# Optimization experiments

Hardware: AMD Instinct MI355X
Metric: run time of the kernel (lower is better)

The kernel has to match this reference:

```python
import jax, jax.numpy as jnp
import numpy as np

E = 1024   # n_embd
H = 16     # n_heads
D = 64     # head_dim
G = 4      # n_kv_groups
F = 4096   # ffn hidden_dim
V = 32000  # vocab
L = 4      # n_layers (all full_attention)
B = 1
T = 2048
ROT = 16   # partial_rotary_factor 0.25 * head_dim 64, rounded to even
EPS = 1e-6
THETA = 10000.0


def rope_tables(seq_len):
    # matches compute_rope_params: inv_freq over even indices of rotary_dim
    inv_freq = 1.0 / (THETA ** (jnp.arange(0, ROT, 2, dtype=jnp.float32) / ROT))
    ang = jnp.arange(seq_len, dtype=jnp.float32)[:, None] * inv_freq[None, :]
    ang = jnp.concatenate([ang, ang], axis=1)  # [T, ROT]
    return jnp.cos(ang), jnp.sin(ang)


def rmsnorm(x, w):
    # torch RMSNorm: x * rsqrt(mean(x^2)+eps) * (1 + weight)
    xf = x.astype(jnp.float32)
    n = xf * jax.lax.rsqrt(jnp.mean(xf * xf, axis=-1, keepdims=True) + EPS)
    return (n * (1.0 + w)).astype(x.dtype)


def apply_rope(x, cos, sin):
    # x: [B, h, T, D]; cos/sin: [1, 1, T, ROT]; partial rotary on first ROT dims
    x_rot, x_pass = x[..., :ROT], x[..., ROT:]
    x1, x2 = x_rot[..., :ROT // 2], x_rot[..., ROT // 2:]
    rotated = jnp.concatenate([-x2, x1], axis=-1)
    return jnp.concatenate([x_rot * cos + rotated * sin, x_pass], axis=-1)


def _forward(tokens, emb, Wq, Wk, Wv, Wo, qn, kn, n1, n2, f1, f2, f3, fn, head):
    cos, sin = rope_tables(T)
    cos = cos[None, None]  # [1,1,T,ROT]
    sin = sin[None, None]
    mask = jnp.triu(jnp.ones((T, T), dtype=bool), k=1)  # True = masked
    scale = D ** -0.5
    x = emb[tokens]  # [B,T,E]

    def block(x, p):
        wq, wk, wv, wo, qw, kw, w1, w2, g1, g2, g3 = p
        h = rmsnorm(x, w1)
        # fused Q + gate projection -> [B,T,H,2D], chunk on last dim
        qg = (h @ wq).reshape(B, T, H, 2 * D)
        q = qg[..., :D].transpose(0, 2, 1, 3)            # [B,H,T,D]
        gate = qg[..., D:].reshape(B, T, H * D)          # [B,T,H*D]
        k = (h @ wk).reshape(B, T, G, D).transpose(0, 2, 1, 3)  # [B,G,T,D]
        v = (h @ wv).reshape(B, T, G, D).transpose(0, 2, 1, 3)
        q = rmsnorm(q, qw)
        k = rmsnorm(k, kw)
        q = apply_rope(q, cos, sin)
        k = apply_rope(k, cos, sin)
        k = jnp.repeat(k, H // G, axis=1)  # GQA expand -> [B,H,T,D]
        v = jnp.repeat(v, H // G, axis=1)
        scores = jnp.einsum('bhqd,bhkd->bhqk', q, k)
        scores = jnp.where(mask, -jnp.inf, scores) * scale
        w = jax.nn.softmax(scores.astype(jnp.float32), axis=-1).astype(q.dtype)
        ctx = jnp.einsum('bhqk,bhkd->bhqd', w, v)
        ctx = ctx.transpose(0, 2, 1, 3).reshape(B, T, H * D)
        ctx = ctx * jax.nn.sigmoid(gate)
        x = x + ctx @ wo
        h2 = rmsnorm(x, w2)
        ff = (jax.nn.silu(h2 @ g1) * (h2 @ g2)) @ g3
        return x + ff, None

    params = (Wq, Wk, Wv, Wo, qn, kn, n1, n2, f1, f2, f3)
    x, _ = jax.lax.scan(block, x, params)
    return rmsnorm(x, fn) @ head  # logits [B,T,V]


def setup_inputs() -> dict:
    key = jax.random.key(0)
    ks = jax.random.split(key, 16)
    s = 0.02
    rn = lambda k, shape, sc=s: jax.random.normal(k, shape, jnp.float32) * sc
    return {
        'tokens': jax.random.randint(ks[0], (B, T), 0, V),
        'emb': rn(ks[1], (V, E)),
        'Wq': rn(ks[2], (L, E, 2 * H * D)),
        'Wk': rn(ks[3], (L, E, G * D)),
        'Wv': rn(ks[4], (L, E, G * D)),
        'Wo': rn(ks[5], (L, H * D, E)),
        'qn': rn(ks[6], (L, D)),
        'kn': rn(ks[7], (L, D)),
        'n1': rn(ks[8], (L, E)),
        'n2': rn(ks[9], (L, E)),
        'f1': rn(ks[10], (L, E, F)),
        'f2': rn(ks[11], (L, E, F)),
        'f3': rn(ks[12], (L, F, E)),
        'fn': rn(ks[13], (E,)),
        'head': rn(ks[14], (E, V)),
    }


def reference(tokens, emb, Wq, Wk, Wv, Wo, qn, kn, n1, n2, f1, f2, f3, fn, head):
    return _forward(tokens, emb, Wq, Wk, Wv, Wo, qn, kn, n1, n2, f1, f2, f3, fn, head)
```

## Files before the change

kernel.cpp:

```cpp
#include <hip/hip_runtime.h>

#define T_LEN 2048
#define E_DIM 1024
#define H_N 16
#define G_N 4
#define D_H 64
#define F_DIM 4096
#define V_SZ 32000
#define L_N 4

typedef __attribute__((ext_vector_type(8))) __bf16 bf16x8;
typedef __attribute__((ext_vector_type(4))) float f32x4;

__device__ __forceinline__ unsigned short f2bf(float f){
  unsigned int u = __float_as_uint(f);
  unsigned int r = (u + 0x7FFFu + ((u >> 16) & 1u)) >> 16;
  return (unsigned short)r;
}

__device__ __forceinline__ f32x4 mfma16(bf16x8 a, bf16x8 b, f32x4 c){
  return __builtin_amdgcn_mfma_f32_16x16x32_bf16(a, b, c, 0, 0, 0);
}

__device__ __forceinline__ void gl16(const void* g, void* l){
  __builtin_amdgcn_global_load_lds((const __attribute__((address_space(1))) void*)g,
                                   (__attribute__((address_space(3))) void*)l, 16, 0, 0);
}

#define SBAR() __builtin_amdgcn_s_barrier()
#define LGK0() do{ asm volatile("s_waitcnt lgkmcnt(0)" ::: "memory"); __builtin_amdgcn_sched_barrier(0); }while(0)
#define VMC4() do{ asm volatile("s_waitcnt vmcnt(4)" ::: "memory"); __builtin_amdgcn_sched_barrier(0); }while(0)
#define VMC0() do{ asm volatile("s_waitcnt vmcnt(0)" ::: "memory"); __builtin_amdgcn_sched_barrier(0); }while(0)

#define QSCALE 0.1803368801111183f

__global__ __launch_bounds__(256) void embed_k(const float* __restrict__ emb,
                                               const int* __restrict__ tokens,
                                               float* __restrict__ x){
  int t = blockIdx.x;
  int tok = tokens[t];
  const float4* src = (const float4*)(emb + (size_t)tok * E_DIM);
  float4* dst = (float4*)(x + (size_t)t * E_DIM);
  dst[threadIdx.x] = src[threadIdx.x];
}

__global__ __launch_bounds__(256) void transpose_bf16(const float* __restrict__ src,
                                                      unsigned short* __restrict__ dst,
                                                      int R, int C){
  __shared__ float tile[32][33];
  int c0 = blockIdx.x * 32, r0 = blockIdx.y * 32;
  int tx = threadIdx.x & 31, ty = threadIdx.x >> 5;
  for (int i = 0; i < 4; i++){
    int r = ty + i * 8;
    tile[r][tx] = src[(size_t)(r0 + r) * C + c0 + tx];
  }
  __syncthreads();
  for (int i = 0; i < 4; i++){
    int r = ty + i * 8;
    dst[(size_t)(c0 + r) * R + r0 + tx] = f2bf(tile[tx][r]);
  }
}

__device__ __forceinline__ void tr32(const float* __restrict__ src, unsigned short* __restrict__ dst,
                                     int R, int C, int bx, int by, float* tile ){
  int c0 = bx * 32, r0 = by * 32;
  int tx = threadIdx.x & 31, ty = threadIdx.x >> 5;
  for (int i = 0; i < 4; i++){
    int r = ty + i * 8;
    tile[r * 33 + tx] = src[(size_t)(r0 + r) * C + c0 + tx];
  }
  __syncthreads();
  for (int i = 0; i < 4; i++){
    int r = ty + i * 8;
    dst[(size_t)(c0 + r) * R + r0 + tx] = f2bf(tile[tx * 33 + r]);
  }
}

__global__ __launch_bounds__(256) void prep_weights(const float* __restrict__ Wq, const float* __restrict__ Wk,
                                                    const float* __restrict__ Wv, const float* __restrict__ Wo,
                                                    const float* __restrict__ f1, const float* __restrict__ f2,
                                                    const float* __restrict__ f3,
                                                    unsigned short* __restrict__ wt_qkv,
                                                    unsigned short* __restrict__ wt_o,
                                                    unsigned short* __restrict__ wt_f12i,
                                                    unsigned short* __restrict__ wt_f3){
  __shared__ float sh[1100];
  int id = blockIdx.x;
  if (id < 2048){ tr32(Wq, wt_qkv, 1024, 2048, id & 63, id >> 6, sh); return; }
  id -= 2048;
  if (id < 256){ tr32(Wk, wt_qkv + 2048 * 1024, 1024, 256, id & 7, id >> 3, sh); return; }
  id -= 256;
  if (id < 256){ tr32(Wv, wt_qkv + 2304 * 1024, 1024, 256, id & 7, id >> 3, sh); return; }
  id -= 256;
  if (id < 1024){ tr32(Wo, wt_o, 1024, 1024, id & 31, id >> 5, sh); return; }
  id -= 1024;
  if (id < 4096){ tr32(f3, wt_f3, 4096, 1024, id & 31, id >> 5, sh); return; }
  id -= 4096;
  {
    int q = id & 255, kb = id >> 8;
    float* t1 = sh; float* t2 = sh + 32 * 17;
    int c = threadIdx.x & 15, kk0 = threadIdx.x >> 4;
    for (int p = 0; p < 2; p++){
      int kk = p * 16 + kk0;
      t1[kk * 17 + c] = f1[(size_t)(kb * 32 + kk) * F_DIM + q * 16 + c];
      t2[kk * 17 + c] = f2[(size_t)(kb * 32 + kk) * F_DIM + q * 16 + c];
    }
    __syncthreads();
    int kk = threadIdx.x & 31, rb = threadIdx.x >> 5;
    for (int i = 0; i < 4; i++){
      int r = i * 8 + rb;
      float v = (r < 16) ? t1[kk * 17 + r] : t2[kk * 17 + (r - 16)];
      wt_f12i[(size_t)(q * 32 + r) * 1024 + kb * 32 + kk] = f2bf(v);
    }
  }
}

__global__ __launch_bounds__(256) void rmsnorm_k(const float* __restrict__ x,
                                                 const float* __restrict__ w,
                                                 unsigned short* __restrict__ out){
  const int t = blockIdx.x, tid = threadIdx.x;
  const float4 v = ((const float4*)(x + (size_t)t * E_DIM))[tid];
  float ss = v.x*v.x + v.y*v.y + v.z*v.z + v.w*v.w;
  for (int m = 1; m < 64; m <<= 1) ss += __shfl_xor(ss, m);
  __shared__ float red[4];
  if ((tid & 63) == 0) red[tid >> 6] = ss;
  __syncthreads();
  ss = red[0] + red[1] + red[2] + red[3];
  const float r = rsqrtf(ss * (1.0f / E_DIM) + 1e-6f);
  const float4 wv = ((const float4*)w)[tid];
  ushort4 o;
  o.x = f2bf(v.x * r * (1.0f + wv.x));
  o.y = f2bf(v.y * r * (1.0f + wv.y));
  o.z = f2bf(v.z * r * (1.0f + wv.z));
  o.w = f2bf(v.w * r * (1.0f + wv.w));
  ((ushort4*)(out + (size_t)t * E_DIM))[tid] = o;
}

template<bool ADD>
__global__ __launch_bounds__(256) void gemm64_bt(const unsigned short* __restrict__ A,
                                                 const unsigned short* __restrict__ Bt,
                                                 float* __restrict__ C,
                                                 int M, int N, int K){
  __shared__ unsigned short As[64 * 32];
  __shared__ unsigned short Bs[128 * 32];
  const int tid = threadIdx.x;
  const int lane = tid & 63, w = tid >> 6;
  const int l15 = lane & 15, l4 = lane >> 4;

  const int chunk = gridDim.x >> 3;
  const int wgid = (blockIdx.x & 7) * chunk + (blockIdx.x >> 3);
  const int nm = M >> 6;
  const int bm = wgid % nm, bn = wgid / nm;
  const int m0 = bm * 64, n0 = bn * 128;

  const int r0 = tid >> 2;
  const int c0 = (tid & 3) << 3;

  const unsigned short* gA  = A  + (size_t)(m0 + r0) * K + c0;
  const unsigned short* gB0 = Bt + (size_t)(n0 + r0) * K + c0;
  const unsigned short* gB1 = Bt + (size_t)(n0 + 64 + r0) * K + c0;
  unsigned short* lA  = As + w * 512;
  unsigned short* lB0 = Bs + w * 512;
  unsigned short* lB1 = Bs + 2048 + w * 512;

  f32x4 acc[4][2] = {};

  for (int k0 = 0; k0 < K; k0 += 32){
    __syncthreads();
    gl16(gA  + k0, lA);
    gl16(gB0 + k0, lB0);
    gl16(gB1 + k0, lB1);
    __syncthreads();
    bf16x8 af[4], bfr[2];
    for (int i = 0; i < 4; i++)
      af[i] = *(const bf16x8*)&As[(i * 16 + l15) * 32 + l4 * 8];
    for (int j = 0; j < 2; j++)
      bfr[j] = *(const bf16x8*)&Bs[(w * 32 + j * 16 + l15) * 32 + l4 * 8];
    for (int i = 0; i < 4; i++)
      for (int j = 0; j < 2; j++)
        acc[i][j] = mfma16(af[i], bfr[j], acc[i][j]);
  }

  for (int i = 0; i < 4; i++)
    for (int j = 0; j < 2; j++){
      int col = n0 + w * 32 + j * 16 + l15;
      for (int r = 0; r < 4; r++){
        int row = m0 + i * 16 + l4 * 4 + r;
        size_t idx = (size_t)row * N + col;
        if (ADD) C[idx] += acc[i][j][r]; else C[idx] = acc[i][j][r];
      }
    }
}

template<int EPI>
__global__ __launch_bounds__(512, 2) void gemm256(const unsigned short* __restrict__ A,
                                                  const unsigned short* __restrict__ Bt,
                                                  float* __restrict__ outF,
                                                  unsigned short* __restrict__ outH,
                                                  int M, int N, int K){
  __shared__ unsigned short lds[65536];
  const int tid = threadIdx.x;
  const int lane = tid & 63, w = tid >> 6;
  const int wm = w >> 2, wn = w & 3;
  const int l15 = lane & 15, l4 = lane >> 4;

  const int chunk = gridDim.x >> 3;
  const int wgid = ((int)blockIdx.x & 7) * chunk + ((int)blockIdx.x >> 3);
  const int nm = M >> 8;
  const int bm = wgid % nm, bn = wgid / nm;
  const int m0 = bm * 256, n0 = bn * 256;
  const int NT = K >> 6;

  const int srow = (lane >> 3);
  const int scol = lane & 7;

  auto stageA = [&](int b, int h, int kt){
    #pragma unroll
    for (int c = 0; c < 2; c++){
      int r = w * 16 + c * 8 + srow;
      const unsigned short* g = A + (size_t)(m0 + h * 128 + r) * K + kt * 64 + ((scol ^ (r & 7)) << 3);
      gl16(g, (char*)lds + (b * 2 + h) * 16384 + (w * 16 + c * 8) * 128);
    }
  };
  auto stageB = [&](int b, int h, int kt){
    #pragma unroll
    for (int c = 0; c < 2; c++){
      int r = w * 16 + c * 8 + srow;
      const unsigned short* g = Bt + (size_t)(n0 + h * 128 + r) * K + kt * 64 + ((scol ^ (r & 7)) << 3);
      gl16(g, (char*)lds + 65536 + (b * 2 + h) * 16384 + (w * 16 + c * 8) * 128);
    }
  };

  const int sl0 = ((l4)     ^ (l15 & 7)) << 4;
  const int sl1 = ((4 | l4) ^ (l15 & 7)) << 4;

  f32x4 acc[8][4] = {};
  bf16x8 aF[8], bF[8];

  stageA(0, 0, 0); stageA(0, 1, 0); stageB(0, 0, 0); stageB(0, 1, 0);
  if (NT > 1){ stageB(1, 0, 1); stageB(1, 1, 1); }
  VMC4();
  SBAR();

  for (int kt = 0; kt < NT; kt++){
    const int buf = kt & 1;
    const char* Ab = (const char*)lds + (buf * 2 + wm) * 16384;
    const char* Bb = (const char*)lds + 65536 + (buf * 2 + (wn >> 1)) * 16384;
    const int brbase = (wn & 1) * 64;

    #pragma unroll
    for (int mf = 0; mf < 4; mf++){
      int r = mf * 16 + l15;
      aF[mf * 2 + 0] = *(const bf16x8*)(Ab + r * 128 + sl0);
      aF[mf * 2 + 1] = *(const bf16x8*)(Ab + r * 128 + sl1);
    }
    #pragma unroll
    for (int nf = 0; nf < 2; nf++){
      int r = brbase + nf * 16 + l15;
      bF[nf * 2 + 0] = *(const bf16x8*)(Bb + r * 128 + sl0);
      bF[nf * 2 + 1] = *(const bf16x8*)(Bb + r * 128 + sl1);
    }
    if (kt + 1 < NT) stageA(buf ^ 1, 0, kt + 1);
    SBAR(); LGK0();
    __builtin_amdgcn_s_setprio(1);
    #pragma unroll
    for (int mf = 0; mf < 4; mf++)
      #pragma unroll
      for (int nf = 0; nf < 2; nf++){
        acc[mf][nf] = mfma16(aF[mf * 2 + 0], bF[nf * 2 + 0], acc[mf][nf]);
        acc[mf][nf] = mfma16(aF[mf * 2 + 1], bF[nf * 2 + 1], acc[mf][nf]);
      }
    __builtin_amdgcn_s_setprio(0);
    SBAR();

    #pragma unroll
    for (int nf = 2; nf < 4; nf++){
      int r = brbase + nf * 16 + l15;
      bF[nf * 2 + 0] = *(const bf16x8*)(Bb + r * 128 + sl0);
      bF[nf * 2 + 1] = *(const bf16x8*)(Bb + r * 128 + sl1);
    }
    if (kt + 1 < NT) stageA(buf ^ 1, 1, kt + 1);
    SBAR(); LGK0();
    __builtin_amdgcn_s_setprio(1);
    #pragma unroll
    for (int mf = 0; mf < 4; mf++)
      #pragma unroll
      for (int nf = 2; nf < 4; nf++){
        acc[mf][nf] = mfma16(aF[mf * 2 + 0], bF[nf * 2 + 0], acc[mf][nf]);
        acc[mf][nf] = mfma16(aF[mf * 2 + 1], bF[nf * 2 + 1], acc[mf][nf]);
      }
    __builtin_amdgcn_s_setprio(0);
    SBAR();

    #pragma unroll
    for (int mf = 0; mf < 4; mf++){
      int r = 64 + mf * 16 + l15;
      aF[mf * 2 + 0] = *(const bf16x8*)(Ab + r * 128 + sl0);
      aF[mf * 2 + 1] = *(const bf16x8*)(Ab + r * 128 + sl1);
    }
    if (kt + 2 < NT) stageB(buf, 0, kt + 2);
    SBAR(); LGK0();
    __builtin_amdgcn_s_setprio(1);
    #pragma unroll
    for (int mf = 0; mf < 4; mf++)
      #pragma unroll
      for (int nf = 2; nf < 4; nf++){
        acc[4 + mf][nf] = mfma16(aF[mf * 2 + 0], bF[nf * 2 + 0], acc[4 + mf][nf]);
        acc[4 + mf][nf] = mfma16(aF[mf * 2 + 1], bF[nf * 2 + 1], acc[4 + mf][nf]);
      }
    __builtin_amdgcn_s_setprio(0);
    SBAR();

    if (kt + 2 < NT) stageB(buf, 1, kt + 2);
    SBAR();
    __builtin_amdgcn_s_setprio(1);
    #pragma unroll
    for (int mf = 0; mf < 4; mf++)
      #pragma unroll
      for (int nf = 0; nf < 2; nf++){
        acc[4 + mf][nf] = mfma16(aF[mf * 2 + 0], bF[nf * 2 + 0], acc[4 + mf][nf]);
        acc[4 + mf][nf] = mfma16(aF[mf * 2 + 1], bF[nf * 2 + 1], acc[4 + mf][nf]);
      }
    __builtin_amdgcn_s_setprio(0);
    if (kt + 2 < NT) { VMC4(); } else { VMC0(); }
    SBAR();
  }

  if (EPI == 0){
    #pragma unroll
    for (int mfg = 0; mfg < 8; mfg++){
      #pragma unroll
      for (int nf = 0; nf < 4; nf++){
        int col = n0 + wn * 64 + nf * 16 + l15;
        int row0 = m0 + wm * 128 + mfg * 16 + l4 * 4;
        #pragma unroll
        for (int r = 0; r < 4; r++)
          outF[(size_t)(row0 + r) * N + col] = acc[mfg][nf][r];
      }
    }
  } else {
    const int NH = N >> 1;
    #pragma unroll
    for (int mfg = 0; mfg < 8; mfg++){
      #pragma unroll
      for (int nfp = 0; nfp < 2; nfp++){
        int col = (n0 >> 1) + wn * 32 + nfp * 16 + l15;
        int row0 = m0 + wm * 128 + mfg * 16 + l4 * 4;
        #pragma unroll
        for (int r = 0; r < 4; r++){
          float u = acc[mfg][nfp * 2 + 0][r];
          float g = acc[mfg][nfp * 2 + 1][r];
          outH[(size_t)(row0 + r) * NH + col] = f2bf(u / (1.0f + __expf(-u)) * g);
        }
      }
    }
  }
}

__global__ __launch_bounds__(256) void qkvpost_k(const float* __restrict__ qkv,
                                                 const float* __restrict__ qn,
                                                 const float* __restrict__ kn,
                                                 unsigned short* __restrict__ qb,
                                                 unsigned short* __restrict__ kb,
                                                 unsigned short* __restrict__ vt){
  const int t = blockIdx.x;
  const int lane = threadIdx.x & 63, w = threadIdx.x >> 6;
  const int d = lane;
  const int fi = d & 7;
  const float invf = powf(10000.0f, -(float)fi * 0.125f);
  const float ang = (float)t * invf;
  const float c = cosf(ang), s = sinf(ang);

  for (int i = 0; i < 4; i++){
    int h = w * 4 + i;
    float v = qkv[(size_t)t * 2560 + h * 128 + d];
    float ss = v * v;
    for (int m = 1; m < 64; m <<= 1) ss += __shfl_xor(ss, m);
    float r = rsqrtf(ss * (1.0f / D_H) + 1e-6f);
    float xn = v * r * (1.0f + qn[d]);
    float partner = __shfl_xor(xn, 8);
    float o;
    if (d < 8)       o = xn * c - partner * s;
    else if (d < 16) o = xn * c + partner * s;
    else             o = xn;
    qb[((size_t)h * T_LEN + t) * D_H + d] = f2bf(o * QSCALE);
  }
  {
    float v = qkv[(size_t)t * 2560 + 2048 + w * 64 + d];
    float ss = v * v;
    for (int m = 1; m < 64; m <<= 1) ss += __shfl_xor(ss, m);
    float r = rsqrtf(ss * (1.0f / D_H) + 1e-6f);
    float xn = v * r * (1.0f + kn[d]);
    float partner = __shfl_xor(xn, 8);
    float o;
    if (d < 8)       o = xn * c - partner * s;
    else if (d < 16) o = xn * c + partner * s;
    else             o = xn;
    kb[((size_t)w * T_LEN + t) * D_H + d] = f2bf(o);
  }
  {
    float v = qkv[(size_t)t * 2560 + 2304 + w * 64 + d];
    vt[((size_t)(w * 64 + d)) * T_LEN + t] = f2bf(v);
  }
}

__global__ __launch_bounds__(64) void attn_k(const unsigned short* __restrict__ qb,
                                             const unsigned short* __restrict__ kb,
                                             const unsigned short* __restrict__ vt,
                                             const float* __restrict__ qkv,
                                             unsigned short* __restrict__ ctxg){
  const int qt = blockIdx.x, h = blockIdx.y;
  const int g = h >> 2;
  const int lane = threadIdx.x;
  const int l15 = lane & 15, l4 = lane >> 4;
  const int q0 = qt * 16;
  __shared__ unsigned short Pl[16][72];

  const bf16x8 aq0 = *(const bf16x8*)(qb + ((size_t)h * T_LEN + q0 + l15) * D_H + l4 * 8);
  const bf16x8 aq1 = *(const bf16x8*)(qb + ((size_t)h * T_LEN + q0 + l15) * D_H + 32 + l4 * 8);

  f32x4 acc[4] = {};
  float mrun[4], lpart[4];
  for (int j = 0; j < 4; j++){ mrun[j] = -1e30f; lpart[j] = 0.0f; }

  for (int kv0 = 0; kv0 <= q0 + 15; kv0 += 64){
    f32x4 sc[4];
    #pragma unroll
    for (int cp = 0; cp < 4; cp++){
      const unsigned short* kbase = kb + ((size_t)g * T_LEN + kv0 + cp * 16 + l15) * D_H + l4 * 8;
      bf16x8 bk0 = *(const bf16x8*)(kbase);
      bf16x8 bk1 = *(const bf16x8*)(kbase + 32);
      f32x4 z = {0.f, 0.f, 0.f, 0.f};
      z = mfma16(aq0, bk0, z);
      z = mfma16(aq1, bk1, z);
      sc[cp] = z;
    }
    float resc[4];
    #pragma unroll
    for (int j = 0; j < 4; j++){
      int r = q0 + l4 * 4 + j;
      #pragma unroll
      for (int cp = 0; cp < 4; cp++){
        int col = kv0 + cp * 16 + l15;
        sc[cp][j] = (col <= r) ? sc[cp][j] : -1e30f;
      }
      float mx = fmaxf(fmaxf(sc[0][j], sc[1][j]), fmaxf(sc[2][j], sc[3][j]));
      for (int off = 1; off < 16; off <<= 1) mx = fmaxf(mx, __shfl_xor(mx, off));
      float mnew = fmaxf(mrun[j], mx);
      resc[j] = exp2f(mrun[j] - mnew);
      mrun[j] = mnew;
      float ssum = 0.0f;
      #pragma unroll
      for (int cp = 0; cp < 4; cp++){
        float pv = exp2f(sc[cp][j] - mnew);
        sc[cp][j] = pv;
        ssum += pv;
      }
      lpart[j] = lpart[j] * resc[j] + ssum;
      #pragma unroll
      for (int nt = 0; nt < 4; nt++) acc[nt][j] *= resc[j];
    }
    __syncthreads();
    #pragma unroll
    for (int j = 0; j < 4; j++)
      #pragma unroll
      for (int cp = 0; cp < 4; cp++)
        Pl[l4 * 4 + j][cp * 16 + l15] = f2bf(sc[cp][j]);
    __syncthreads();
    const bf16x8 pa0 = *(const bf16x8*)&Pl[l15][l4 * 8];
    const bf16x8 pa1 = *(const bf16x8*)&Pl[l15][32 + l4 * 8];
    #pragma unroll
    for (int nt = 0; nt < 4; nt++){
      const unsigned short* vbase = vt + ((size_t)g * 64 + nt * 16 + l15) * T_LEN + kv0;
      bf16x8 bv0 = *(const bf16x8*)(vbase + l4 * 8);
      bf16x8 bv1 = *(const bf16x8*)(vbase + 32 + l4 * 8);
      acc[nt] = mfma16(pa1, bv1, mfma16(pa0, bv0, acc[nt]));
    }
  }

  #pragma unroll
  for (int j = 0; j < 4; j++)
    for (int off = 1; off < 16; off <<= 1) lpart[j] += __shfl_xor(lpart[j], off);

  #pragma unroll
  for (int j = 0; j < 4; j++){
    int r = q0 + l4 * 4 + j;
    float inv = 1.0f / lpart[j];
    #pragma unroll
    for (int nt = 0; nt < 4; nt++){
      int d = nt * 16 + l15;
      float gate = qkv[(size_t)r * 2560 + h * 128 + 64 + d];
      float val = acc[nt][j] * inv * (1.0f / (1.0f + __expf(-gate)));
      ctxg[(size_t)r * (H_N * D_H) + h * D_H + d] = f2bf(val);
    }
  }
}

extern "C" void kernel_launch(void* const* d_in, const int* in_sizes, int n_in,
                              void* d_out, int out_size, void* d_ws, size_t ws_size,
                              hipStream_t stream){
  (void)in_sizes; (void)n_in; (void)out_size; (void)ws_size;
  const int*   tokens = (const int*)d_in[0];
  const float* emb    = (const float*)d_in[1];
  const float* Wq     = (const float*)d_in[2];
  const float* Wk     = (const float*)d_in[3];
  const float* Wv     = (const float*)d_in[4];
  const float* Wo     = (const float*)d_in[5];
  const float* qn     = (const float*)d_in[6];
  const float* kn     = (const float*)d_in[7];
  const float* n1     = (const float*)d_in[8];
  const float* n2     = (const float*)d_in[9];
  const float* f1     = (const float*)d_in[10];
  const float* f2     = (const float*)d_in[11];
  const float* f3     = (const float*)d_in[12];
  const float* fn     = (const float*)d_in[13];
  const float* head   = (const float*)d_in[14];
  float* out = (float*)d_out;

  char* ws = (char*)d_ws;
  size_t off = 0;
  auto alloc = [&](size_t bytes)->char*{
    char* p = ws + off;
    off += (bytes + 255) & ~(size_t)255;
    return p;
  };
  float*          x       = (float*)alloc((size_t)T_LEN * E_DIM * 4);
  unsigned short* hbf     = (unsigned short*)alloc((size_t)T_LEN * E_DIM * 2);
  float*          qkvf    = (float*)alloc((size_t)T_LEN * 2560 * 4);
  unsigned short* qb      = (unsigned short*)alloc((size_t)H_N * T_LEN * D_H * 2);
  unsigned short* kb      = (unsigned short*)alloc((size_t)G_N * T_LEN * D_H * 2);
  unsigned short* vt      = (unsigned short*)alloc((size_t)G_N * D_H * T_LEN * 2);
  unsigned short* ctxg    = (unsigned short*)alloc((size_t)T_LEN * E_DIM * 2);
  unsigned short* hg      = (unsigned short*)alloc((size_t)T_LEN * F_DIM * 2);
  unsigned short* wt_qkv  = (unsigned short*)alloc((size_t)2560 * E_DIM * 2);
  unsigned short* wt_o    = (unsigned short*)alloc((size_t)E_DIM * E_DIM * 2);
  unsigned short* wt_f12i = (unsigned short*)alloc((size_t)2 * F_DIM * E_DIM * 2);
  unsigned short* wt_f3   = (unsigned short*)alloc((size_t)E_DIM * F_DIM * 2);
  unsigned short* wt_head = (unsigned short*)alloc((size_t)V_SZ * E_DIM * 2);

  embed_k<<<T_LEN, 256, 0, stream>>>(emb, tokens, x);
  transpose_bf16<<<dim3(V_SZ / 32, E_DIM / 32), 256, 0, stream>>>(head, wt_head, E_DIM, V_SZ);

  for (int l = 0; l < L_N; l++){
    prep_weights<<<15872, 256, 0, stream>>>(Wq + (size_t)l * E_DIM * 2048,
                                            Wk + (size_t)l * E_DIM * 256,
                                            Wv + (size_t)l * E_DIM * 256,
                                            Wo + (size_t)l * E_DIM * E_DIM,
                                            f1 + (size_t)l * E_DIM * F_DIM,
                                            f2 + (size_t)l * E_DIM * F_DIM,
                                            f3 + (size_t)l * F_DIM * E_DIM,
                                            wt_qkv, wt_o, wt_f12i, wt_f3);

    rmsnorm_k<<<T_LEN, 256, 0, stream>>>(x, n1 + l * E_DIM, hbf);
    gemm64_bt<false><<<(T_LEN / 64) * (2560 / 128), 256, 0, stream>>>(hbf, wt_qkv, qkvf, T_LEN, 2560, E_DIM);
    qkvpost_k<<<T_LEN, 256, 0, stream>>>(qkvf, qn + l * D_H, kn + l * D_H, qb, kb, vt);
    attn_k<<<dim3(T_LEN / 16, H_N), 64, 0, stream>>>(qb, kb, vt, qkvf, ctxg);
    gemm64_bt<true><<<(T_LEN / 64) * (E_DIM / 128), 256, 0, stream>>>(ctxg, wt_o, x, T_LEN, E_DIM, E_DIM);

    rmsnorm_k<<<T_LEN, 256, 0, stream>>>(x, n2 + l * E_DIM, hbf);
    gemm256<1><<<(T_LEN / 256) * (2 * F_DIM / 256), 512, 0, stream>>>(hbf, wt_f12i, nullptr, hg, T_LEN, 2 * F_DIM, E_DIM);
    gemm64_bt<true><<<(T_LEN / 64) * (E_DIM / 128), 256, 0, stream>>>(hg, wt_f3, x, T_LEN, E_DIM, F_DIM);
  }

  rmsnorm_k<<<T_LEN, 256, 0, stream>>>(x, fn, hbf);
  gemm256<0><<<(T_LEN / 256) * (V_SZ / 256), 512, 0, stream>>>(hbf, wt_head, out, nullptr, T_LEN, V_SZ, E_DIM);
}
```

Measured before the change: 1.569 ms.

## Split attention KV into chunks with combine kernel; rebalance XCD mapping

The causal attention kernel now splits each query tile's KV range into chunks of 256 positions along a third grid dimension. Each chunk writes unnormalized partial outputs plus running max and sum to workspace, and a new combine kernel merges them and applies the sigmoid gate. This is meant to remove the load imbalance of long causal rows and expose more blocks, at the cost of an extra launch and extra global traffic for the partials. The gemm256 XCD remap now handles grid sizes that are not a multiple of 8, and the LM-head GEMM is split into two launches of 63 and 62 column tiles.

```diff
diff --git a/kernel.cpp b/kernel.cpp
--- a/kernel.cpp
+++ b/kernel.cpp
@@ -204,8 +204,10 @@
   const int wm = w >> 2, wn = w & 3;
   const int l15 = lane & 15, l4 = lane >> 4;
 
-  const int chunk = gridDim.x >> 3;
-  const int wgid = ((int)blockIdx.x & 7) * chunk + ((int)blockIdx.x >> 3);
+  const int nwg = gridDim.x;
+  const int xcd = (int)blockIdx.x & 7, lin = (int)blockIdx.x >> 3;
+  const int q8 = nwg >> 3, r8 = nwg & 7;
+  const int wgid = (xcd < r8 ? xcd * (q8 + 1) : r8 * (q8 + 1) + (xcd - r8) * q8) + lin;
   const int nm = M >> 8;
   const int bm = wgid % nm, bn = wgid / nm;
   const int m0 = bm * 256, n0 = bn * 256;
@@ -407,13 +409,18 @@
 __global__ __launch_bounds__(64) void attn_k(const unsigned short* __restrict__ qb,
                                              const unsigned short* __restrict__ kb,
                                              const unsigned short* __restrict__ vt,
-                                             const float* __restrict__ qkv,
-                                             unsigned short* __restrict__ ctxg){
-  const int qt = blockIdx.x, h = blockIdx.y;
+                                             float* __restrict__ po,
+                                             float* __restrict__ pm,
+                                             float* __restrict__ pl){
+  const int qt = blockIdx.x, h = blockIdx.y, c = blockIdx.z;
+  const int nch = (qt >> 4) + 1;
+  if (c >= nch) return;
   const int g = h >> 2;
   const int lane = threadIdx.x;
   const int l15 = lane & 15, l4 = lane >> 4;
   const int q0 = qt * 16;
+  const int kvbeg = c << 8;
+  const int kvend = min(kvbeg + 256, q0 + 16);
   __shared__ unsigned short Pl[16][72];
 
   const bf16x8 aq0 = *(const bf16x8*)(qb + ((size_t)h * T_LEN + q0 + l15) * D_H + l4 * 8);
@@ -423,7 +430,7 @@
   float mrun[4], lpart[4];
   for (int j = 0; j < 4; j++){ mrun[j] = -1e30f; lpart[j] = 0.0f; }
 
-  for (int kv0 = 0; kv0 <= q0 + 15; kv0 += 64){
+  for (int kv0 = kvbeg; kv0 < kvend; kv0 += 64){
     f32x4 sc[4];
     #pragma unroll
     for (int cp = 0; cp < 4; cp++){
@@ -482,17 +489,46 @@
   for (int j = 0; j < 4; j++)
     for (int off = 1; off < 16; off <<= 1) lpart[j] += __shfl_xor(lpart[j], off);
 
+  const int pidx = ((h << 7) + qt) * 8 + c;
+  float* poB = po + (size_t)pidx * (16 * 64);
   #pragma unroll
   for (int j = 0; j < 4; j++){
-    int r = q0 + l4 * 4 + j;
-    float inv = 1.0f / lpart[j];
-    #pragma unroll
-    for (int nt = 0; nt < 4; nt++){
-      int d = nt * 16 + l15;
-      float gate = qkv[(size_t)r * 2560 + h * 128 + 64 + d];
-      float val = acc[nt][j] * inv * (1.0f / (1.0f + __expf(-gate)));
-      ctxg[(size_t)r * (H_N * D_H) + h * D_H + d] = f2bf(val);
-    }
+    int row = l4 * 4 + j;
+    #pragma unroll
+    for (int nt = 0; nt < 4; nt++)
+      poB[row * 64 + nt * 16 + l15] = acc[nt][j];
+  }
+  if (l15 == 0){
+    #pragma unroll
+    for (int j = 0; j < 4; j++){
+      pm[pidx * 16 + l4 * 4 + j] = mrun[j];
+      pl[pidx * 16 + l4 * 4 + j] = lpart[j];
+    }
+  }
+}
+
+__global__ __launch_bounds__(64) void attn_combine(const float* __restrict__ po,
+                                                   const float* __restrict__ pm,
+                                                   const float* __restrict__ pl,
+                                                   const float* __restrict__ qkv,
+                                                   unsigned short* __restrict__ ctxg){
+  const int qt = blockIdx.x, h = blockIdx.y;
+  const int nch = (qt >> 4) + 1;
+  const int d = threadIdx.x;
+  const int q0 = qt << 4;
+  const int base = ((h << 7) + qt) * 8;
+  for (int r = 0; r < 16; r++){
+    float mstar = -1e30f;
+    for (int c = 0; c < nch; c++) mstar = fmaxf(mstar, pm[(base + c) * 16 + r]);
+    float accv = 0.f, lsum = 0.f;
+    for (int c = 0; c < nch; c++){
+      float wgt = exp2f(pm[(base + c) * 16 + r] - mstar);
+      accv += wgt * po[(size_t)(base + c) * 1024 + r * 64 + d];
+      lsum += wgt * pl[(base + c) * 16 + r];
+    }
+    float gate = qkv[(size_t)(q0 + r) * 2560 + h * 128 + 64 + d];
+    float val = accv / lsum * (1.0f / (1.0f + __expf(-gate)));
+    ctxg[(size_t)(q0 + r) * (H_N * D_H) + h * D_H + d] = f2bf(val);
   }
 }
 
@@ -532,6 +568,9 @@
   unsigned short* vt      = (unsigned short*)alloc((size_t)G_N * D_H * T_LEN * 2);
   unsigned short* ctxg    = (unsigned short*)alloc((size_t)T_LEN * E_DIM * 2);
   unsigned short* hg      = (unsigned short*)alloc((size_t)T_LEN * F_DIM * 2);
+  float*          po      = (float*)alloc((size_t)H_N * 128 * 8 * 16 * 64 * 4);
+  float*          pm      = (float*)alloc((size_t)H_N * 128 * 8 * 16 * 4);
+  float*          pl      = (float*)alloc((size_t)H_N * 128 * 8 * 16 * 4);
   unsigned short* wt_qkv  = (unsigned short*)alloc((size_t)2560 * E_DIM * 2);
   unsigned short* wt_o    = (unsigned short*)alloc((size_t)E_DIM * E_DIM * 2);
   unsigned short* wt_f12i = (unsigned short*)alloc((size_t)2 * F_DIM * E_DIM * 2);
@@ -554,7 +593,8 @@
     rmsnorm_k<<<T_LEN, 256, 0, stream>>>(x, n1 + l * E_DIM, hbf);
     gemm64_bt<false><<<(T_LEN / 64) * (2560 / 128), 256, 0, stream>>>(hbf, wt_qkv, qkvf, T_LEN, 2560, E_DIM);
     qkvpost_k<<<T_LEN, 256, 0, stream>>>(qkvf, qn + l * D_H, kn + l * D_H, qb, kb, vt);
-    attn_k<<<dim3(T_LEN / 16, H_N), 64, 0, stream>>>(qb, kb, vt, qkvf, ctxg);
+    attn_k<<<dim3(T_LEN / 16, H_N, 8), 64, 0, stream>>>(qb, kb, vt, po, pm, pl);
+    attn_combine<<<dim3(T_LEN / 16, H_N), 64, 0, stream>>>(po, pm, pl, qkvf, ctxg);
     gemm64_bt<true><<<(T_LEN / 64) * (E_DIM / 128), 256, 0, stream>>>(ctxg, wt_o, x, T_LEN, E_DIM, E_DIM);
 
     rmsnorm_k<<<T_LEN, 256, 0, stream>>>(x, n2 + l * E_DIM, hbf);
@@ -563,5 +603,7 @@
   }
 
   rmsnorm_k<<<T_LEN, 256, 0, stream>>>(x, fn, hbf);
-  gemm256<0><<<(T_LEN / 256) * (V_SZ / 256), 512, 0, stream>>>(hbf, wt_head, out, nullptr, T_LEN, V_SZ, E_DIM);
-}
+  gemm256<0><<<(T_LEN / 256) * 63, 512, 0, stream>>>(hbf, wt_head, out, nullptr, T_LEN, V_SZ, E_DIM);
+  gemm256<0><<<(T_LEN / 256) * 62, 512, 0, stream>>>(hbf, wt_head + (size_t)(63 * 256) * E_DIM,
+                                                     out + (size_t)(63 * 256), nullptr, T_LEN, V_SZ, E_DIM);
+}
```

New measurement: 1.644 ms. 1.05x slower.

## Split attention KV chunks across four waves with LDS softmax merge

Applied to the files above, without the earlier changes.

The attention kernel grows from one wave to four waves per 16-row query tile. Each wave handles every fourth 64-wide KV chunk with its own online softmax, and the partial outputs, maxima and sums are merged through shared memory before gating and storing. This gives more parallelism on long causal rows, which were processed serially by a single wave, and removes the block-wide barriers around the P staging buffer. The cost is extra LDS traffic and a final reduction. The GEMM XCD block remap is also generalised to grid sizes that are not multiples of eight.

```diff
diff --git a/kernel.cpp b/kernel.cpp
--- a/kernel.cpp
+++ b/kernel.cpp
@@ -204,8 +204,10 @@
   const int wm = w >> 2, wn = w & 3;
   const int l15 = lane & 15, l4 = lane >> 4;
 
-  const int chunk = gridDim.x >> 3;
-  const int wgid = ((int)blockIdx.x & 7) * chunk + ((int)blockIdx.x >> 3);
+  const int nwg = gridDim.x;
+  const int xcd = (int)blockIdx.x & 7, lin = (int)blockIdx.x >> 3;
+  const int q8 = nwg >> 3, r8 = nwg & 7;
+  const int wgid = (xcd < r8 ? xcd * (q8 + 1) : r8 * (q8 + 1) + (xcd - r8) * q8) + lin;
   const int nm = M >> 8;
   const int bm = wgid % nm, bn = wgid / nm;
   const int m0 = bm * 256, n0 = bn * 256;
@@ -404,26 +406,35 @@
   }
 }
 
-__global__ __launch_bounds__(64) void attn_k(const unsigned short* __restrict__ qb,
-                                             const unsigned short* __restrict__ kb,
-                                             const unsigned short* __restrict__ vt,
-                                             const float* __restrict__ qkv,
-                                             unsigned short* __restrict__ ctxg){
+__global__ __launch_bounds__(256) void attn_k(const unsigned short* __restrict__ qb,
+                                              const unsigned short* __restrict__ kb,
+                                              const unsigned short* __restrict__ vt,
+                                              const float* __restrict__ qkv,
+                                              unsigned short* __restrict__ ctxg){
   const int qt = blockIdx.x, h = blockIdx.y;
   const int g = h >> 2;
-  const int lane = threadIdx.x;
+  const int tid = threadIdx.x;
+  const int wv = tid >> 6;
+  const int lane = tid & 63;
   const int l15 = lane & 15, l4 = lane >> 4;
   const int q0 = qt * 16;
-  __shared__ unsigned short Pl[16][72];
+  const int nch = (q0 >> 6) + 1;
+
+  __shared__ unsigned short Pl[4][16][72];
+  __shared__ float sO[4][16][66];
+  __shared__ float sM[4][16];
+  __shared__ float sL[4][16];
 
   const bf16x8 aq0 = *(const bf16x8*)(qb + ((size_t)h * T_LEN + q0 + l15) * D_H + l4 * 8);
   const bf16x8 aq1 = *(const bf16x8*)(qb + ((size_t)h * T_LEN + q0 + l15) * D_H + 32 + l4 * 8);
 
   f32x4 acc[4] = {};
   float mrun[4], lpart[4];
+  #pragma unroll
   for (int j = 0; j < 4; j++){ mrun[j] = -1e30f; lpart[j] = 0.0f; }
 
-  for (int kv0 = 0; kv0 <= q0 + 15; kv0 += 64){
+  for (int c = wv; c < nch; c += 4){
+    const int kv0 = c << 6;
     f32x4 sc[4];
     #pragma unroll
     for (int cp = 0; cp < 4; cp++){
@@ -460,15 +471,14 @@
       #pragma unroll
       for (int nt = 0; nt < 4; nt++) acc[nt][j] *= resc[j];
     }
-    __syncthreads();
     #pragma unroll
     for (int j = 0; j < 4; j++)
       #pragma unroll
       for (int cp = 0; cp < 4; cp++)
-        Pl[l4 * 4 + j][cp * 16 + l15] = f2bf(sc[cp][j]);
-    __syncthreads();
-    const bf16x8 pa0 = *(const bf16x8*)&Pl[l15][l4 * 8];
-    const bf16x8 pa1 = *(const bf16x8*)&Pl[l15][32 + l4 * 8];
+        Pl[wv][l4 * 4 + j][cp * 16 + l15] = f2bf(sc[cp][j]);
+    asm volatile("s_waitcnt lgkmcnt(0)" ::: "memory");
+    const bf16x8 pa0 = *(const bf16x8*)&Pl[wv][l15][l4 * 8];
+    const bf16x8 pa1 = *(const bf16x8*)&Pl[wv][l15][32 + l4 * 8];
     #pragma unroll
     for (int nt = 0; nt < 4; nt++){
       const unsigned short* vbase = vt + ((size_t)g * 64 + nt * 16 + l15) * T_LEN + kv0;
@@ -484,15 +494,31 @@
 
   #pragma unroll
   for (int j = 0; j < 4; j++){
-    int r = q0 + l4 * 4 + j;
-    float inv = 1.0f / lpart[j];
-    #pragma unroll
-    for (int nt = 0; nt < 4; nt++){
-      int d = nt * 16 + l15;
-      float gate = qkv[(size_t)r * 2560 + h * 128 + 64 + d];
-      float val = acc[nt][j] * inv * (1.0f / (1.0f + __expf(-gate)));
-      ctxg[(size_t)r * (H_N * D_H) + h * D_H + d] = f2bf(val);
-    }
+    int row = l4 * 4 + j;
+    #pragma unroll
+    for (int nt = 0; nt < 4; nt++)
+      sO[wv][row][nt * 16 + l15] = acc[nt][j];
+  }
+  if (l15 == 0){
+    #pragma unroll
+    for (int j = 0; j < 4; j++){
+      sM[wv][l4 * 4 + j] = mrun[j];
+      sL[wv][l4 * 4 + j] = lpart[j];
+    }
+  }
+  __syncthreads();
+
+  #pragma unroll
+  for (int rr = 0; rr < 4; rr++){
+    int r = wv * 4 + rr;
+    float m0 = sM[0][r], m1 = sM[1][r], m2 = sM[2][r], m3 = sM[3][r];
+    float ms = fmaxf(fmaxf(m0, m1), fmaxf(m2, m3));
+    float w0 = exp2f(m0 - ms), w1 = exp2f(m1 - ms), w2 = exp2f(m2 - ms), w3 = exp2f(m3 - ms);
+    float accv = w0 * sO[0][r][lane] + w1 * sO[1][r][lane] + w2 * sO[2][r][lane] + w3 * sO[3][r][lane];
+    float lsum = w0 * sL[0][r] + w1 * sL[1][r] + w2 * sL[2][r] + w3 * sL[3][r];
+    float gate = qkv[(size_t)(q0 + r) * 2560 + h * 128 + 64 + lane];
+    float val = accv / lsum * (1.0f / (1.0f + __expf(-gate)));
+    ctxg[(size_t)(q0 + r) * (H_N * D_H) + h * D_H + lane] = f2bf(val);
   }
 }
 
@@ -554,7 +580,7 @@
     rmsnorm_k<<<T_LEN, 256, 0, stream>>>(x, n1 + l * E_DIM, hbf);
     gemm64_bt<false><<<(T_LEN / 64) * (2560 / 128), 256, 0, stream>>>(hbf, wt_qkv, qkvf, T_LEN, 2560, E_DIM);
     qkvpost_k<<<T_LEN, 256, 0, stream>>>(qkvf, qn + l * D_H, kn + l * D_H, qb, kb, vt);
-    attn_k<<<dim3(T_LEN / 16, H_N), 64, 0, stream>>>(qb, kb, vt, qkvf, ctxg);
+    attn_k<<<dim3(T_LEN / 16, H_N), 256, 0, stream>>>(qb, kb, vt, qkvf, ctxg);
     gemm64_bt<true><<<(T_LEN / 64) * (E_DIM / 128), 256, 0, stream>>>(ctxg, wt_o, x, T_LEN, E_DIM, E_DIM);
 
     rmsnorm_k<<<T_LEN, 256, 0, stream>>>(x, n2 + l * E_DIM, hbf);
```

Measured after the change: 1.412 ms. 10.0% less time.
